# Kernel tuning notes

Measured on AMD Instinct MI355X. Metric: run time of the kernel, lower is better.

The kernel has to match this reference:

```python
import jax, jax.numpy as jnp
import numpy as np

NBOXES = 4096
MAX_BS = 128
NDIM = 3
NPAIRS = 8192
INV4PI = 0.07957747154594767  # 1/(4*pi), 3D Laplace kernel constant


def setup_inputs() -> dict:
    key = jax.random.key(0)
    k1, k2, k3, k4 = jax.random.split(key, 4)
    q_vec = jax.random.normal(k1, (NBOXES, MAX_BS), dtype=jnp.float32)
    XX_list = jax.random.uniform(k2, (NBOXES, MAX_BS, NDIM), dtype=jnp.float32)
    bs_list = jax.random.randint(k3, (NBOXES,), 0, MAX_BS, dtype=jnp.int32)
    uq_boxes = jax.random.randint(k4, (NPAIRS, 2), 0, NBOXES, dtype=jnp.int32)
    return {"q_vec": q_vec, "XX_list": XX_list, "bs_list": bs_list, "uq_boxes": uq_boxes}


def reference(q_vec, XX_list, bs_list, uq_boxes):
    # Batched gather-kernel-matvec-scatter translation (addto_translation with
    # self_bool=False, kappa=0 => 3D Laplace kernel 1/(4*pi*r)).
    nboxes, max_bs = q_vec.shape
    u_boxes = uq_boxes[:, 0]
    q_boxes = uq_boxes[:, 1]

    Xu = XX_list[u_boxes]  # [P, B, 3] gather target points
    Xq = XX_list[q_boxes]  # [P, B, 3] gather source points

    # pairwise squared distances without materializing [P,B,B,3] diffs
    nu = jnp.sum(Xu * Xu, axis=-1)  # [P, B]
    nq = jnp.sum(Xq * Xq, axis=-1)  # [P, B]
    r2 = nu[:, :, None] + nq[:, None, :] - 2.0 * jnp.einsum('pid,pjd->pij', Xu, Xq)
    r2 = jnp.maximum(r2, 0.0)
    nz = r2 > 0.0
    K = jnp.where(nz, INV4PI / jnp.sqrt(jnp.where(nz, r2, 1.0)), 0.0)  # [P, B, B]

    cols = jnp.arange(max_bs, dtype=jnp.int32)
    col_mask = (cols[None, :] < bs_list[q_boxes][:, None]).astype(q_vec.dtype)  # valid src pts
    row_mask = (cols[None, :] < bs_list[u_boxes][:, None]).astype(q_vec.dtype)  # valid trg pts

    qv = q_vec[q_boxes] * col_mask                         # gather + zero_col_bnd
    out = jnp.einsum('pij,pj->pi', K, qv) * row_mask       # batched kernel matvec

    u_vec = jnp.zeros_like(q_vec).at[u_boxes].add(out)     # index_add_ scatter
    return u_vec
```

## Files before the change

### kernel.cpp

```cpp
#include <hip/hip_runtime.h>

#define NBOXES 4096
#define MAX_BS 128
#define INV4PI 0.07957747154594767f

__global__ __launch_bounds__(128) void fmm_pair_kernel(
    const float* __restrict__ q_vec,
    const float* __restrict__ XX,
    const int*   __restrict__ bs_list,
    const int2*  __restrict__ uq_boxes,
    float*       __restrict__ out)
{
    const int p = blockIdx.x;
    const int t = threadIdx.x;

    const int2 uq = uq_boxes[p];
    const int u = uq.x;
    const int q = uq.y;
    const int bs_u = bs_list[u];
    const int bs_q = bs_list[q];

    __shared__ float4 sq[MAX_BS];

    {
        const float* Xq = XX + (size_t)q * (MAX_BS * 3);
        float x = Xq[3 * t + 0];
        float y = Xq[3 * t + 1];
        float z = Xq[3 * t + 2];
        float w = (t < bs_q) ? q_vec[(size_t)q * MAX_BS + t] * INV4PI : 0.0f;
        sq[t] = make_float4(x, y, z, w);
    }

    const float* Xu = XX + (size_t)u * (MAX_BS * 3);
    const float xu = Xu[3 * t + 0];
    const float yu = Xu[3 * t + 1];
    const float zu = Xu[3 * t + 2];

    __syncthreads();

    if (t >= bs_u) return;

    float acc = 0.0f;
    const int n = bs_q;
#pragma unroll 4
    for (int j = 0; j < n; ++j) {
        const float4 s = sq[j];
        const float dx = xu - s.x;
        const float dy = yu - s.y;
        const float dz = zu - s.z;
        const float r2 = dx * dx + dy * dy + dz * dz;
        float rinv = __builtin_amdgcn_rsqf(r2);
        rinv = (r2 > 0.0f) ? rinv : 0.0f;
        acc = fmaf(s.w, rinv, acc);
    }

    atomicAdd(out + (size_t)u * MAX_BS + t, acc);
}

extern "C" void kernel_launch(void* const* d_in, const int* in_sizes, int n_in,
                              void* d_out, int out_size, void* d_ws, size_t ws_size,
                              hipStream_t stream) {
    const float* q_vec    = (const float*)d_in[0];
    const float* XX_list  = (const float*)d_in[1];
    const int*   bs_list  = (const int*)d_in[2];
    const int2*  uq_boxes = (const int2*)d_in[3];
    float* out = (float*)d_out;

    const int npairs = in_sizes[3] / 2;

    hipMemsetAsync(d_out, 0, (size_t)out_size * sizeof(float), stream);

    fmm_pair_kernel<<<npairs, 128, 0, stream>>>(q_vec, XX_list, bs_list,
                                                uq_boxes, out);
}
```

Before: 89.15 us.

## Bin pairs by target box and accumulate per-box without atomics

Adds a binning kernel that groups source boxes by target box into a fixed-capacity list, then launches one block per target box that loops over its sources and writes the result directly. This removes the global atomic scatter and the output memset, and keeps target points in registers across pairs. In exchange it adds a launch, a barrier per source box, and load imbalance across target boxes. A target with more than CAP source pairs would silently drop work.

New measurement: 114.9 us. 28.9% more time.

```diff
diff --git a/kernel.cpp b/kernel.cpp
--- a/kernel.cpp
+++ b/kernel.cpp
@@ -3,58 +3,76 @@
 #define NBOXES 4096
 #define MAX_BS 128
 #define INV4PI 0.07957747154594767f
+#define CAP 512
 
-__global__ __launch_bounds__(128) void fmm_pair_kernel(
+__global__ __launch_bounds__(256) void bin_pairs_kernel(
+    const int2* __restrict__ uq_boxes, int npairs,
+    int* __restrict__ cnt,
+    int* __restrict__ qlist)
+{
+    int p = blockIdx.x * 256 + threadIdx.x;
+    if (p >= npairs) return;
+    int2 uq = uq_boxes[p];
+    int slot = atomicAdd(&cnt[uq.x], 1);
+    if (slot < CAP) qlist[(size_t)uq.x * CAP + slot] = uq.y;
+}
+
+__global__ __launch_bounds__(128) void fmm_gather_kernel(
     const float* __restrict__ q_vec,
     const float* __restrict__ XX,
     const int*   __restrict__ bs_list,
-    const int2*  __restrict__ uq_boxes,
+    const int*   __restrict__ cnt,
+    const int*   __restrict__ qlist,
     float*       __restrict__ out)
 {
-    const int p = blockIdx.x;
+    const int u = blockIdx.x;
     const int t = threadIdx.x;
 
-    const int2 uq = uq_boxes[p];
-    const int u = uq.x;
-    const int q = uq.y;
     const int bs_u = bs_list[u];
-    const int bs_q = bs_list[q];
-
-    __shared__ float4 sq[MAX_BS];
-
-    {
-        const float* Xq = XX + (size_t)q * (MAX_BS * 3);
-        float x = Xq[3 * t + 0];
-        float y = Xq[3 * t + 1];
-        float z = Xq[3 * t + 2];
-        float w = (t < bs_q) ? q_vec[(size_t)q * MAX_BS + t] * INV4PI : 0.0f;
-        sq[t] = make_float4(x, y, z, w);
-    }
+    int npq = cnt[u];
+    if (npq > CAP) npq = CAP;
 
     const float* Xu = XX + (size_t)u * (MAX_BS * 3);
     const float xu = Xu[3 * t + 0];
     const float yu = Xu[3 * t + 1];
     const float zu = Xu[3 * t + 2];
 
-    __syncthreads();
+    __shared__ float4 sq[MAX_BS];
 
-    if (t >= bs_u) return;
+    const int wbase = t & 64;
+    float acc = 0.0f;
 
-    float acc = 0.0f;
-    const int n = bs_q;
+    for (int k = 0; k < npq; ++k) {
+        int q = __builtin_amdgcn_readfirstlane(qlist[(size_t)u * CAP + k]);
+        const int bs_q = bs_list[q];
+
+        __syncthreads();
+        {
+            const float* Xq = XX + (size_t)q * (MAX_BS * 3);
+            float x = Xq[3 * t + 0];
+            float y = Xq[3 * t + 1];
+            float z = Xq[3 * t + 2];
+            float w = (t < bs_q) ? q_vec[(size_t)q * MAX_BS + t] * INV4PI : 0.0f;
+            sq[t] = make_float4(x, y, z, w);
+        }
+        __syncthreads();
+
+        if (wbase < bs_u) {
 #pragma unroll 4
-    for (int j = 0; j < n; ++j) {
-        const float4 s = sq[j];
-        const float dx = xu - s.x;
-        const float dy = yu - s.y;
-        const float dz = zu - s.z;
-        const float r2 = dx * dx + dy * dy + dz * dz;
-        float rinv = __builtin_amdgcn_rsqf(r2);
-        rinv = (r2 > 0.0f) ? rinv : 0.0f;
-        acc = fmaf(s.w, rinv, acc);
+            for (int j = 0; j < bs_q; ++j) {
+                const float4 s = sq[j];
+                const float dx = xu - s.x;
+                const float dy = yu - s.y;
+                const float dz = zu - s.z;
+                const float r2 = dx * dx + dy * dy + dz * dz;
+                float rinv = __builtin_amdgcn_rsqf(r2);
+                rinv = (r2 > 0.0f) ? rinv : 0.0f;
+                acc = fmaf(s.w, rinv, acc);
+            }
+        }
     }
 
-    atomicAdd(out + (size_t)u * MAX_BS + t, acc);
+    out[(size_t)u * MAX_BS + t] = (t < bs_u) ? acc : 0.0f;
 }
 
 extern "C" void kernel_launch(void* const* d_in, const int* in_sizes, int n_in,
@@ -68,8 +86,14 @@
 
     const int npairs = in_sizes[3] / 2;
 
-    hipMemsetAsync(d_out, 0, (size_t)out_size * sizeof(float), stream);
+    int* cnt   = (int*)d_ws;
+    int* qlist = (int*)d_ws + NBOXES;
 
-    fmm_pair_kernel<<<npairs, 128, 0, stream>>>(q_vec, XX_list, bs_list,
-                                                uq_boxes, out);
+    hipMemsetAsync(cnt, 0, NBOXES * sizeof(int), stream);
+
+    bin_pairs_kernel<<<(npairs + 255) / 256, 256, 0, stream>>>(
+        uq_boxes, npairs, cnt, qlist);
+
+    fmm_gather_kernel<<<NBOXES, 128, 0, stream>>>(
+        q_vec, XX_list, bs_list, cnt, qlist, out);
 }
```

## Map one wavefront per box pair with two target rows per lane

Applied to the files above, without the earlier changes.

Each 128-thread block now handles two pairs, one 64-lane wavefront each, and every lane computes up to two target points. Depending on bs_u, a one-row or two-row sweep runs over the source points, reading them from LDS in groups of eight. The aim is to reuse each LDS source load across two targets, skip the second row when the target box is small, and avoid idle lanes in partially filled boxes. The cost is more serial work per wavefront and twice as many pairs per block. It assumes npairs is even.

Result: slower. 93.16 us (+4.5%).

```diff
diff --git a/kernel.cpp b/kernel.cpp
--- a/kernel.cpp
+++ b/kernel.cpp
@@ -4,15 +4,58 @@
 #define MAX_BS 128
 #define INV4PI 0.07957747154594767f
 
-__global__ __launch_bounds__(128) void fmm_pair_kernel(
+template<int NR>
+__device__ __forceinline__ void sweep(const float4* __restrict__ sq, int bs_q,
+                                      const float* xu, const float* yu,
+                                      const float* zu, float* acc)
+{
+    int j = 0;
+    for (; j + 8 <= bs_q; j += 8) {
+        float4 s[8];
+#pragma unroll
+        for (int c = 0; c < 8; ++c) s[c] = sq[j + c];
+#pragma unroll
+        for (int c = 0; c < 8; ++c) {
+#pragma unroll
+            for (int r = 0; r < NR; ++r) {
+                const float dx = xu[r] - s[c].x;
+                const float dy = yu[r] - s[c].y;
+                const float dz = zu[r] - s[c].z;
+                const float r2 = dx * dx + dy * dy + dz * dz;
+                float rinv = __builtin_amdgcn_rsqf(r2);
+                rinv = (r2 > 0.0f) ? rinv : 0.0f;
+                acc[r] = fmaf(s[c].w, rinv, acc[r]);
+            }
+        }
+    }
+    for (; j < bs_q; ++j) {
+        const float4 s = sq[j];
+#pragma unroll
+        for (int r = 0; r < NR; ++r) {
+            const float dx = xu[r] - s.x;
+            const float dy = yu[r] - s.y;
+            const float dz = zu[r] - s.z;
+            const float r2 = dx * dx + dy * dy + dz * dz;
+            float rinv = __builtin_amdgcn_rsqf(r2);
+            rinv = (r2 > 0.0f) ? rinv : 0.0f;
+            acc[r] = fmaf(s.w, rinv, acc[r]);
+        }
+    }
+}
+
+__global__ __launch_bounds__(128) void fmm_pair2_kernel(
     const float* __restrict__ q_vec,
     const float* __restrict__ XX,
     const int*   __restrict__ bs_list,
     const int2*  __restrict__ uq_boxes,
+    int npairs,
     float*       __restrict__ out)
 {
-    const int p = blockIdx.x;
-    const int t = threadIdx.x;
+    const int w = threadIdx.x >> 6;
+    const int t = threadIdx.x & 63;
+    const int p = blockIdx.x * 2 + w;
+
+    __shared__ float4 sq[2][MAX_BS];
 
     const int2 uq = uq_boxes[p];
     const int u = uq.x;
@@ -20,41 +63,42 @@
     const int bs_u = bs_list[u];
     const int bs_q = bs_list[q];
 
-    __shared__ float4 sq[MAX_BS];
-
     {
         const float* Xq = XX + (size_t)q * (MAX_BS * 3);
-        float x = Xq[3 * t + 0];
-        float y = Xq[3 * t + 1];
-        float z = Xq[3 * t + 2];
-        float w = (t < bs_q) ? q_vec[(size_t)q * MAX_BS + t] * INV4PI : 0.0f;
-        sq[t] = make_float4(x, y, z, w);
+        const float* qv = q_vec + (size_t)q * MAX_BS;
+#pragma unroll
+        for (int r = 0; r < 2; ++r) {
+            const int jj = t + 64 * r;
+            const float x = Xq[3 * jj + 0];
+            const float y = Xq[3 * jj + 1];
+            const float z = Xq[3 * jj + 2];
+            const float wt = (jj < bs_q) ? qv[jj] * INV4PI : 0.0f;
+            sq[w][jj] = make_float4(x, y, z, wt);
+        }
     }
 
     const float* Xu = XX + (size_t)u * (MAX_BS * 3);
-    const float xu = Xu[3 * t + 0];
-    const float yu = Xu[3 * t + 1];
-    const float zu = Xu[3 * t + 2];
+    float xu[2], yu[2], zu[2];
+#pragma unroll
+    for (int r = 0; r < 2; ++r) {
+        const int ii = t + 64 * r;
+        xu[r] = Xu[3 * ii + 0];
+        yu[r] = Xu[3 * ii + 1];
+        zu[r] = Xu[3 * ii + 2];
+    }
 
     __syncthreads();
 
-    if (t >= bs_u) return;
-
-    float acc = 0.0f;
-    const int n = bs_q;
-#pragma unroll 4
-    for (int j = 0; j < n; ++j) {
-        const float4 s = sq[j];
-        const float dx = xu - s.x;
-        const float dy = yu - s.y;
-        const float dz = zu - s.z;
-        const float r2 = dx * dx + dy * dy + dz * dz;
-        float rinv = __builtin_amdgcn_rsqf(r2);
-        rinv = (r2 > 0.0f) ? rinv : 0.0f;
-        acc = fmaf(s.w, rinv, acc);
+    float acc[2] = {0.0f, 0.0f};
+    if (bs_u > 64) {
+        sweep<2>(sq[w], bs_q, xu, yu, zu, acc);
+    } else if (bs_u > 0) {
+        sweep<1>(sq[w], bs_q, xu, yu, zu, acc);
     }
 
-    atomicAdd(out + (size_t)u * MAX_BS + t, acc);
+    float* orow = out + (size_t)u * MAX_BS;
+    if (t < bs_u)      atomicAdd(orow + t,      acc[0]);
+    if (t + 64 < bs_u) atomicAdd(orow + t + 64, acc[1]);
 }
 
 extern "C" void kernel_launch(void* const* d_in, const int* in_sizes, int n_in,
@@ -70,6 +114,6 @@
 
     hipMemsetAsync(d_out, 0, (size_t)out_size * sizeof(float), stream);
 
-    fmm_pair_kernel<<<npairs, 128, 0, stream>>>(q_vec, XX_list, bs_list,
-                                                uq_boxes, out);
+    fmm_pair2_kernel<<<npairs / 2, 128, 0, stream>>>(
+        q_vec, XX_list, bs_list, uq_boxes, npairs, out);
 }
```

## Use persistent blocks with register prefetch and double-buffered shared sources

Applied to the files above, without the earlier changes.

Replaces the one-block-per-pair launch with a fixed grid of 2048 blocks that loop over pairs in a grid-stride pattern. Each block loads the next pair's source and target points into registers while computing the current pair, alternating between two shared-memory buffers. The goal is to hide global gather latency and cut block launch overhead. It also drops the r2>0 guard when the two boxes differ. That relies on points from different boxes never coinciding, since a coincident pair would make rsq return inf and give a wrong or NaN sum.

After: 92.49 us. 3.7% more time.

```diff
diff --git a/kernel.cpp b/kernel.cpp
--- a/kernel.cpp
+++ b/kernel.cpp
@@ -1,60 +1,88 @@
 #include <hip/hip_runtime.h>
 
-#define NBOXES 4096
 #define MAX_BS 128
 #define INV4PI 0.07957747154594767f
+#define GRID 2048
 
-__global__ __launch_bounds__(128) void fmm_pair_kernel(
+__global__ __launch_bounds__(128) void fmm_persist_kernel(
     const float* __restrict__ q_vec,
     const float* __restrict__ XX,
     const int*   __restrict__ bs_list,
     const int2*  __restrict__ uq_boxes,
+    int npairs, int iters,
     float*       __restrict__ out)
 {
-    const int p = blockIdx.x;
-    const int t = threadIdx.x;
+    const int i = threadIdx.x;
+    __shared__ float4 sq[2][MAX_BS];
 
-    const int2 uq = uq_boxes[p];
-    const int u = uq.x;
-    const int q = uq.y;
-    const int bs_u = bs_list[u];
-    const int bs_q = bs_list[q];
+    int p = blockIdx.x;
 
-    __shared__ float4 sq[MAX_BS];
-
-    {
+    int u = 0, q = 0, bs_u = 0, bs_q = 0;
+    float sx = 0.f, sy = 0.f, sz = 0.f, sw = 0.f;
+    float xu = 0.f, yu = 0.f, zu = 0.f;
+    if (p < npairs) {
+        const int2 uq = uq_boxes[p];
+        u = uq.x; q = uq.y;
+        bs_u = bs_list[u]; bs_q = bs_list[q];
         const float* Xq = XX + (size_t)q * (MAX_BS * 3);
-        float x = Xq[3 * t + 0];
-        float y = Xq[3 * t + 1];
-        float z = Xq[3 * t + 2];
-        float w = (t < bs_q) ? q_vec[(size_t)q * MAX_BS + t] * INV4PI : 0.0f;
-        sq[t] = make_float4(x, y, z, w);
+        sx = Xq[3 * i + 0]; sy = Xq[3 * i + 1]; sz = Xq[3 * i + 2];
+        sw = q_vec[(size_t)q * MAX_BS + i];
+        const float* Xu = XX + (size_t)u * (MAX_BS * 3);
+        xu = Xu[3 * i + 0]; yu = Xu[3 * i + 1]; zu = Xu[3 * i + 2];
     }
 
-    const float* Xu = XX + (size_t)u * (MAX_BS * 3);
-    const float xu = Xu[3 * t + 0];
-    const float yu = Xu[3 * t + 1];
-    const float zu = Xu[3 * t + 2];
+    for (int it = 0; it < iters; ++it) {
+        const int buf = it & 1;
+        sq[buf][i] = make_float4(sx, sy, sz,
+                                 (i < bs_q) ? sw * INV4PI : 0.0f);
+        __syncthreads();
 
-    __syncthreads();
+        const int   cu = u, cbs_u = bs_u, cbs_q = bs_q;
+        const bool  self  = (u == q);
+        const bool  valid = (p < npairs);
+        const float cxu = xu, cyu = yu, czu = zu;
 
-    if (t >= bs_u) return;
+        p += GRID;
+        if (it + 1 < iters && p < npairs) {
+            const int2 uq = uq_boxes[p];
+            u = uq.x; q = uq.y;
+            bs_u = bs_list[u]; bs_q = bs_list[q];
+            const float* Xq = XX + (size_t)q * (MAX_BS * 3);
+            sx = Xq[3 * i + 0]; sy = Xq[3 * i + 1]; sz = Xq[3 * i + 2];
+            sw = q_vec[(size_t)q * MAX_BS + i];
+            const float* Xu = XX + (size_t)u * (MAX_BS * 3);
+            xu = Xu[3 * i + 0]; yu = Xu[3 * i + 1]; zu = Xu[3 * i + 2];
+        }
 
-    float acc = 0.0f;
-    const int n = bs_q;
+        if (valid && i < cbs_u) {
+            const float4* __restrict__ s = sq[buf];
+            float acc = 0.0f;
+            if (self) {
 #pragma unroll 4
-    for (int j = 0; j < n; ++j) {
-        const float4 s = sq[j];
-        const float dx = xu - s.x;
-        const float dy = yu - s.y;
-        const float dz = zu - s.z;
-        const float r2 = dx * dx + dy * dy + dz * dz;
-        float rinv = __builtin_amdgcn_rsqf(r2);
-        rinv = (r2 > 0.0f) ? rinv : 0.0f;
-        acc = fmaf(s.w, rinv, acc);
+                for (int j = 0; j < cbs_q; ++j) {
+                    const float4 sj = s[j];
+                    const float dx = cxu - sj.x;
+                    const float dy = cyu - sj.y;
+                    const float dz = czu - sj.z;
+                    const float r2 = dx * dx + dy * dy + dz * dz;
+                    float rinv = __builtin_amdgcn_rsqf(r2);
+                    rinv = (r2 > 0.0f) ? rinv : 0.0f;
+                    acc = fmaf(sj.w, rinv, acc);
+                }
+            } else {
+#pragma unroll 4
+                for (int j = 0; j < cbs_q; ++j) {
+                    const float4 sj = s[j];
+                    const float dx = cxu - sj.x;
+                    const float dy = cyu - sj.y;
+                    const float dz = czu - sj.z;
+                    const float r2 = dx * dx + dy * dy + dz * dz;
+                    acc = fmaf(sj.w, __builtin_amdgcn_rsqf(r2), acc);
+                }
+            }
+            atomicAdd(out + (size_t)cu * MAX_BS + i, acc);
+        }
     }
-
-    atomicAdd(out + (size_t)u * MAX_BS + t, acc);
 }
 
 extern "C" void kernel_launch(void* const* d_in, const int* in_sizes, int n_in,
@@ -67,9 +95,10 @@
     float* out = (float*)d_out;
 
     const int npairs = in_sizes[3] / 2;
+    const int iters  = (npairs + GRID - 1) / GRID;
 
     hipMemsetAsync(d_out, 0, (size_t)out_size * sizeof(float), stream);
 
-    fmm_pair_kernel<<<npairs, 128, 0, stream>>>(q_vec, XX_list, bs_list,
-                                                uq_boxes, out);
+    fmm_persist_kernel<<<GRID, 128, 0, stream>>>(
+        q_vec, XX_list, bs_list, uq_boxes, npairs, iters, out);
 }
```
